# Kernel tuning notes

Measured on AMD Instinct MI355X. Metric: run time of the kernel, lower is better.

Reference implementation:

```python
import jax, jax.numpy as jnp
import numpy as np

SPACE = 63
STRIDE = 2
TEMP = 0.07
W_CHAR, W_WORD, W_PHRASE, W_IDEA = 1.0, 0.5, 0.1, 0.1


def setup_inputs() -> dict:
    key = jax.random.key(0)
    ks = jax.random.split(key, 6)
    B, S, V, D = 8, 4096, 256, 512
    return {
        "logits": jax.random.normal(ks[0], (B, S, V), jnp.float32),
        "word_preds": jax.random.normal(ks[1], (B, D, S // STRIDE), jnp.float32),
        "char_features": jax.random.normal(ks[2], (B, D, S), jnp.float32),
        "contrastive_2": jax.random.normal(ks[3], (B, 128, 1024), jnp.float32),
        "contrastive_3": jax.random.normal(ks[4], (B, 128, 256), jnp.float32),
        "targets": jax.random.randint(ks[5], (B, S), 0, V, jnp.int32),
        "mask": jnp.ones((B, S), jnp.float32),
    }


def _info_nce(emb, temp=TEMP):
    # emb: (B, dim, L). Anchors = even positions, positives = odd positions.
    B, dim, L = emb.shape
    n_pairs = L // 2
    a = emb[:, :, 0:2 * n_pairs:2].transpose(0, 2, 1).reshape(-1, dim)
    p = emb[:, :, 1:2 * n_pairs:2].transpose(0, 2, 1).reshape(-1, dim)
    a = a / jnp.maximum(jnp.linalg.norm(a, axis=1, keepdims=True), 1e-12)
    p = p / jnp.maximum(jnp.linalg.norm(p, axis=1, keepdims=True), 1e-12)
    logits = (a @ p.T) / temp  # (n, n)
    n = logits.shape[0]
    logp = jax.nn.log_softmax(logits, axis=1)
    idx = jnp.arange(n)
    return -jnp.mean(logp[idx, idx])


def _word_span_loss(word_preds, char_features, targets, stride=STRIDE):
    # Segment-mean over spans between consecutive spaces; MSE vs gathered preds.
    B, D, S = char_features.shape
    Wlen = word_preds.shape[2]
    nseg = S + 2  # segment k in [1, n_spaces-1] = span after the k-th space; last slot = junk
    space = targets == SPACE
    cs = jnp.cumsum(space.astype(jnp.int32), axis=1)  # inclusive space count
    seg = jnp.where(space, nseg - 1, cs)          # non-space chars -> span id
    seg_sp = jnp.where(space, cs, nseg - 1)       # space positions -> their space index k
    t_idx = jnp.arange(S, dtype=jnp.int32)

    def per_batch(feats, seg_b, seg_sp_b):
        sums = jax.ops.segment_sum(feats.T, seg_b, num_segments=nseg)  # (nseg, D)
        cnts = jax.ops.segment_sum(jnp.ones((S,), feats.dtype), seg_b, num_segments=nseg)
        pos = jnp.full((nseg,), S, jnp.int32).at[seg_sp_b].set(t_idx)  # position of k-th space
        return sums, cnts, pos

    sums, cnts, pos = jax.vmap(per_batch)(char_features, seg, seg_sp)
    n_sp = cs[:, -1]  # (B,)
    k = jnp.arange(nseg)[None, :]
    valid = (k >= 1) & (k <= n_sp[:, None] - 1) & (cnts > 0) & ((pos // stride) < Wlen)
    means = jax.lax.stop_gradient(sums / jnp.maximum(cnts, 1.0)[..., None])  # target.detach()
    wp = jnp.clip(pos // stride, 0, Wlen - 1)  # (B, nseg)
    preds = jnp.take_along_axis(word_preds.transpose(0, 2, 1), wp[:, :, None], axis=1)  # (B,nseg,D)
    mse = jnp.mean((preds - means) ** 2, axis=-1)  # per-span F.mse_loss (mean over feat dim)
    tot = jnp.sum(jnp.where(valid, mse, 0.0))
    cnt = jnp.sum(valid).astype(mse.dtype)
    return jnp.where(cnt > 0, tot / jnp.maximum(cnt, 1.0), 0.0)


def reference(logits, word_preds, char_features, contrastive_2, contrastive_3, targets, mask):
    # char CE with mask
    logp = jax.nn.log_softmax(logits, axis=-1)
    ce = -jnp.take_along_axis(logp, targets[..., None].astype(jnp.int32), axis=-1)[..., 0]
    n = jnp.sum(mask)
    char_loss = jnp.where(n > 0, jnp.sum(ce * mask) / jnp.maximum(n, 1.0), jnp.mean(ce))
    word_loss = _word_span_loss(word_preds, char_features, targets)
    phrase_loss = _info_nce(contrastive_2)
    idea_loss = _info_nce(contrastive_3)
    return (W_CHAR * char_loss + W_WORD * word_loss
            + W_PHRASE * phrase_loss + W_IDEA * idea_loss)
```

## Files before the change

kernel.cpp:

```cpp
#include <hip/hip_runtime.h>

#define SPACE_TOK 63
#define INV_T 14.285714285714286f
#define SA_SCALE 20.609929155556595f
#define LN2F 0.6931471805599453f

typedef __attribute__((ext_vector_type(8))) short bf16x8;
typedef __attribute__((ext_vector_type(4))) float f32x4;

#define O_CECM   0
#define O_CEM    4096
#define O_CEC    8192
#define O_WPART  12288
#define O_WCNT   14336
#define O_PEXP2  14464
#define O_DIAG2  145536
#define O_PEXP3  161920
#define O_DIAG3  194688
#define O_A2     198848
#define SZ_A2    (4096*128*2)
#define O_P2     (O_A2 + SZ_A2)
#define O_A3     (O_P2 + SZ_A2)
#define SZ_A3    (1024*128*2)
#define O_P3     (O_A3 + SZ_A3)

#define SMEM_A   18048
#define NTILE    4
#define SMEM_NCE (4*64*17*4 + 4*64*4)

__device__ inline unsigned short f2bf(float x) {
  union { float f; unsigned int u; } c; c.f = x;
  unsigned int r = c.u + 0x7fffu + ((c.u >> 16) & 1u);
  return (unsigned short)(r >> 16);
}

__device__ void norm_body(char* smem, const float* __restrict__ emb, int L,
                          unsigned short* __restrict__ Abf, unsigned short* __restrict__ Pbf,
                          int b, int l0) {
  float (*tile)[33] = (float(*)[33])smem;
  float (*np8)[32]  = (float(*)[32])(smem + 16896);
  float* scl        = (float*)(smem + 16896 + 1024);
  int tid = threadIdx.x;
  int lx = tid & 31, cq = tid >> 5;
  const float* eb = emb + (size_t)b * 128 * L + l0;
  for (int c = cq; c < 128; c += 8) tile[c][lx] = eb[(size_t)c * L + lx];
  __syncthreads();
  {
    float s = 0.f;
    for (int c = cq; c < 128; c += 8) { float x = tile[c][lx]; s += x * x; }
    np8[cq][lx] = s;
  }
  __syncthreads();
  if (tid < 32) {
    float t = 0.f;
#pragma unroll
    for (int g = 0; g < 8; ++g) t += np8[g][tid];
    float nrm = fmaxf(sqrtf(t), 1e-12f);
    scl[tid] = ((tid & 1) ? 1.0f : SA_SCALE) / nrm;
  }
  __syncthreads();
  int c = tid & 127, lh = tid >> 7;
  int half = L >> 1;
  int k = c >> 5, quad = (c >> 3) & 3, j = c & 7;
  for (int lp = lh; lp < 32; lp += 2) {
    int l = l0 + lp;
    int row = b * half + (l >> 1);
    unsigned short v = f2bf(tile[c][lp] * scl[lp]);
    unsigned short* dst = (l & 1) ? Pbf : Abf;
    dst[(size_t)(row >> 4) * 2048 + k * 512 + ((quad << 4) + (row & 15)) * 8 + j] = v;
  }
}

__device__ void word_body(char* smem, const float* __restrict__ wp,
                          const float* __restrict__ cf,
                          const int* __restrict__ targets,
                          char* __restrict__ ws, int w) {
  int* sc      = (int*)smem;
  int* splist  = (int*)(smem + 1024);
  int* snext_sh = (int*)(smem + 5120);
  float* wacc  = (float*)(smem + 5124);
  int tid = threadIdx.x;
  int z = w & 15, tq = (w >> 4) & 3, b = w >> 6;
  const int* tb = targets + b * 4096;
  int tbase = tq * 1024;
  int4 tok = ((const int4*)(tb + tbase))[tid];
  int f0 = (tok.x == SPACE_TOK), f1 = (tok.y == SPACE_TOK),
      f2 = (tok.z == SPACE_TOK), f3 = (tok.w == SPACE_TOK);
  int cnt = f0 + f1 + f2 + f3;
  sc[tid] = cnt;
  __syncthreads();
  for (int off = 1; off < 256; off <<= 1) {
    int v = (tid >= off) ? sc[tid - off] : 0;
    __syncthreads();
    sc[tid] += v;
    __syncthreads();
  }
  int base = sc[tid] - cnt;
  int p = tbase + tid * 4;
  if (f0) splist[base++] = p;
  if (f1) splist[base++] = p + 1;
  if (f2) splist[base++] = p + 2;
  if (f3) splist[base++] = p + 3;
  int m = sc[255];
  if (tid == 0) *snext_sh = -1;
  __syncthreads();
  if (m > 0) {
    for (int wstart = tbase + 1024; wstart < 4096 && *snext_sh < 0; wstart += 1024) {
      int t = wstart + tid * 4;
      int4 tk = ((const int4*)tb)[t >> 2];
      int found = 0x7fffffff;
      if (tk.x == SPACE_TOK) found = t;
      else if (tk.y == SPACE_TOK) found = t + 1;
      else if (tk.z == SPACE_TOK) found = t + 2;
      else if (tk.w == SPACE_TOK) found = t + 3;
#pragma unroll
      for (int mm = 1; mm < 64; mm <<= 1) found = min(found, __shfl_xor(found, mm));
      if ((tid & 63) == 0) sc[tid >> 6] = found;
      __syncthreads();
      if (tid == 0) {
        int f = min(min(sc[0], sc[1]), min(sc[2], sc[3]));
        if (f != 0x7fffffff) *snext_sh = f;
      }
      __syncthreads();
    }
  }
  int snext = *snext_sh;
  int wave = tid >> 6, lane = tid & 63;
  int dbase = z * 32 + wave * 8;
  const float* r0 = cf + ((size_t)(b * 512 + dbase)) * 4096;
  float myacc = 0.f;
  float lcnt = 0.f;
  for (int i = 0; i < m; ++i) {
    int t0 = splist[i];
    int t1 = (i + 1 < m) ? splist[i + 1] : snext;
    if (t1 < 0) break;
    int seglen = t1 - t0 - 1;
    if (seglen <= 0) continue;
    lcnt += 1.0f;
    int wpos = t0 >> 1;
    float invc = 1.0f / (float)seglen;
    float pred = 0.f;
    if (lane < 8) pred = wp[((size_t)(b * 512 + dbase + lane)) * 2048 + wpos];
    int c0 = (t0 + 1) >> 2;
    int c1 = (t1 + 3) >> 2;
    float s0 = 0.f, s1 = 0.f, s2 = 0.f, s3 = 0.f, s4 = 0.f, s5 = 0.f, s6 = 0.f, s7 = 0.f;
    for (int c = c0 + lane; c < c1; c += 64) {
      int tbp = c << 2;
      float4 v0 = *(const float4*)(r0 + 0 * 4096 + tbp);
      float4 v1 = *(const float4*)(r0 + 1 * 4096 + tbp);
      float4 v2 = *(const float4*)(r0 + 2 * 4096 + tbp);
      float4 v3 = *(const float4*)(r0 + 3 * 4096 + tbp);
      float4 v4 = *(const float4*)(r0 + 4 * 4096 + tbp);
      float4 v5 = *(const float4*)(r0 + 5 * 4096 + tbp);
      float4 v6 = *(const float4*)(r0 + 6 * 4096 + tbp);
      float4 v7 = *(const float4*)(r0 + 7 * 4096 + tbp);
      float m0 = (tbp + 0 > t0 && tbp + 0 < t1) ? 1.f : 0.f;
      float m1 = (tbp + 1 > t0 && tbp + 1 < t1) ? 1.f : 0.f;
      float m2 = (tbp + 2 > t0 && tbp + 2 < t1) ? 1.f : 0.f;
      float m3 = (tbp + 3 > t0 && tbp + 3 < t1) ? 1.f : 0.f;
      s0 += v0.x * m0 + v0.y * m1 + v0.z * m2 + v0.w * m3;
      s1 += v1.x * m0 + v1.y * m1 + v1.z * m2 + v1.w * m3;
      s2 += v2.x * m0 + v2.y * m1 + v2.z * m2 + v2.w * m3;
      s3 += v3.x * m0 + v3.y * m1 + v3.z * m2 + v3.w * m3;
      s4 += v4.x * m0 + v4.y * m1 + v4.z * m2 + v4.w * m3;
      s5 += v5.x * m0 + v5.y * m1 + v5.z * m2 + v5.w * m3;
      s6 += v6.x * m0 + v6.y * m1 + v6.z * m2 + v6.w * m3;
      s7 += v7.x * m0 + v7.y * m1 + v7.z * m2 + v7.w * m3;
    }
#pragma unroll
    for (int mm = 1; mm < 64; mm <<= 1) {
      s0 += __shfl_xor(s0, mm); s1 += __shfl_xor(s1, mm);
      s2 += __shfl_xor(s2, mm); s3 += __shfl_xor(s3, mm);
      s4 += __shfl_xor(s4, mm); s5 += __shfl_xor(s5, mm);
      s6 += __shfl_xor(s6, mm); s7 += __shfl_xor(s7, mm);
    }
    if (lane < 8) {
      float sv = (lane == 0) ? s0 : (lane == 1) ? s1 : (lane == 2) ? s2 : (lane == 3) ? s3
               : (lane == 4) ? s4 : (lane == 5) ? s5 : (lane == 6) ? s6 : s7;
      float mean = sv * invc;
      float diff = pred - mean;
      myacc += diff * diff;
    }
  }
#pragma unroll
  for (int mm = 1; mm < 8; mm <<= 1) myacc += __shfl_xor(myacc, mm);
  if (lane == 0) wacc[wave] = myacc;
  __syncthreads();
  if (tid == 0) {
    ((float*)(ws + O_WPART))[w] = (wacc[0] + wacc[1] + wacc[2] + wacc[3]) * (1.0f / 512.0f);
    if (z == 0) ((float*)(ws + O_WCNT))[w >> 4] = lcnt;
  }
}

__device__ void ce_body(char* smem, const float* __restrict__ logits,
                        const int* __restrict__ targets, const float* __restrict__ mask,
                        char* ws, int cb) {
  int tid = threadIdx.x;
  int wave = tid >> 6, lane = tid & 63;
  int rbase = cb * 32 + wave * 8;
  float4 v[8];
  float mk[8];
  int tg[8];
#pragma unroll
  for (int rr = 0; rr < 8; ++rr) v[rr] = ((const float4*)logits)[(size_t)(rbase + rr) * 64 + lane];
#pragma unroll
  for (int rr = 0; rr < 8; ++rr) { tg[rr] = targets[rbase + rr]; mk[rr] = mask[rbase + rr]; }
  float aCM = 0.f, aM = 0.f, aC = 0.f;
#pragma unroll
  for (int rr = 0; rr < 8; ++rr) {
    float e = __expf(v[rr].x) + __expf(v[rr].y) + __expf(v[rr].z) + __expf(v[rr].w);
#pragma unroll
    for (int m = 1; m < 64; m <<= 1) e += __shfl_xor(e, m);
    int t = tg[rr];
    int q = t & 3;
    float sel = (q == 0) ? v[rr].x : (q == 1) ? v[rr].y : (q == 2) ? v[rr].z : v[rr].w;
    float xt = __shfl(sel, t >> 2);
    float ce = __logf(e) - xt;
    aCM += ce * mk[rr]; aM += mk[rr]; aC += ce;
  }
  float (*red)[3] = (float(*)[3])smem;
  if (lane == 0) { red[wave][0] = aCM; red[wave][1] = aM; red[wave][2] = aC; }
  __syncthreads();
  if (tid == 0) {
    ((float*)(ws + O_CECM))[cb] = red[0][0] + red[1][0] + red[2][0] + red[3][0];
    ((float*)(ws + O_CEM ))[cb] = red[0][1] + red[1][1] + red[2][1] + red[3][1];
    ((float*)(ws + O_CEC ))[cb] = red[0][2] + red[1][2] + red[2][2] + red[3][2];
  }
}

__global__ void __launch_bounds__(256) fusedA_kernel(const float* __restrict__ logits,
                                                     const float* __restrict__ wp,
                                                     const float* __restrict__ cf,
                                                     const int* __restrict__ targets,
                                                     const float* __restrict__ mask,
                                                     const float* __restrict__ c2,
                                                     const float* __restrict__ c3,
                                                     char* __restrict__ ws) {
  extern __shared__ char smem[];
  int bid = blockIdx.x;
  if (bid < 512) {
    word_body(smem, wp, cf, targets, ws, bid);
  } else if (bid < 1536) {
    ce_body(smem, logits, targets, mask, ws, bid - 512);
  } else if (bid < 1792) {
    int nb = bid - 1536;
    norm_body(smem, c2, 1024, (unsigned short*)(ws + O_A2), (unsigned short*)(ws + O_P2),
              nb & 7, (nb >> 3) * 32);
  } else {
    int nb = bid - 1792;
    norm_body(smem, c3, 256, (unsigned short*)(ws + O_A3), (unsigned short*)(ws + O_P3),
              nb & 7, (nb >> 3) * 32);
  }
}

__device__ void nce_body(char* smem, const unsigned short* __restrict__ A,
                         const unsigned short* __restrict__ P, int sliceJ,
                         int grp, int s, float* __restrict__ pexp,
                         float* __restrict__ diag) {
  int tid = threadIdx.x;
  int wave = tid >> 6, lane = tid & 63;
  int col = lane & 15, quad = lane >> 4;
  int I0g = grp * (16 * NTILE);
  const unsigned short* At = A + (size_t)(I0g >> 4) * 2048 + lane * 8;
  bf16x8 a[NTILE][4];
#pragma unroll
  for (int t = 0; t < NTILE; ++t)
#pragma unroll
    for (int k = 0; k < 4; ++k)
      a[t][k] = *(const bf16x8*)(At + t * 2048 + k * 512);
  float rl[NTILE][4];
#pragma unroll
  for (int t = 0; t < NTILE; ++t)
#pragma unroll
    for (int q = 0; q < 4; ++q) rl[t][q] = 0.f;
  float dcap[NTILE];
#pragma unroll
  for (int t = 0; t < NTILE; ++t) dcap[t] = 0.f;
  int perW = sliceJ >> 2;
  int J0w = s * sliceJ + wave * perW, Jend = J0w + perW;
  for (int J = J0w; J < Jend; J += 16) {
    const unsigned short* Pt = P + (size_t)(J >> 4) * 2048 + lane * 8;
    bf16x8 b0 = *(const bf16x8*)(Pt);
    bf16x8 b1 = *(const bf16x8*)(Pt + 512);
    bf16x8 b2 = *(const bf16x8*)(Pt + 1024);
    bf16x8 b3 = *(const bf16x8*)(Pt + 1536);
#pragma unroll
    for (int t = 0; t < NTILE; ++t) {
      f32x4 cfr = {0.f, 0.f, 0.f, 0.f};
      cfr = __builtin_amdgcn_mfma_f32_16x16x32_bf16(a[t][0], b0, cfr, 0, 0, 0);
      cfr = __builtin_amdgcn_mfma_f32_16x16x32_bf16(a[t][1], b1, cfr, 0, 0, 0);
      cfr = __builtin_amdgcn_mfma_f32_16x16x32_bf16(a[t][2], b2, cfr, 0, 0, 0);
      cfr = __builtin_amdgcn_mfma_f32_16x16x32_bf16(a[t][3], b3, cfr, 0, 0, 0);
      rl[t][0] += exp2f(cfr[0] - SA_SCALE);
      rl[t][1] += exp2f(cfr[1] - SA_SCALE);
      rl[t][2] += exp2f(cfr[2] - SA_SCALE);
      rl[t][3] += exp2f(cfr[3] - SA_SCALE);
      if (J == I0g + 16 * t) {
        int r = col - (quad << 2);
        if (r == 0) dcap[t] = cfr[0];
        else if (r == 1) dcap[t] = cfr[1];
        else if (r == 2) dcap[t] = cfr[2];
        else if (r == 3) dcap[t] = cfr[3];
      }
    }
  }
  float (*part)[64][17] = (float(*)[64][17])smem;
  float (*dpart)[64]    = (float(*)[64])(smem + 18496);
#pragma unroll
  for (int t = 0; t < NTILE; ++t) {
    part[wave][t * 16 + (quad << 2) + 0][col] = rl[t][0];
    part[wave][t * 16 + (quad << 2) + 1][col] = rl[t][1];
    part[wave][t * 16 + (quad << 2) + 2][col] = rl[t][2];
    part[wave][t * 16 + (quad << 2) + 3][col] = rl[t][3];
    if (quad == (col >> 2)) dpart[wave][t * 16 + col] = dcap[t];
  }
  __syncthreads();
  {
    int rrow = tid >> 4, cc = tid & 15;
#pragma unroll
    for (int t = 0; t < NTILE; ++t) {
      int row = t * 16 + rrow;
      float sv = 0.f, d = 0.f;
#pragma unroll
      for (int ww = 0; ww < 4; ++ww) { sv += part[ww][row][cc]; d += dpart[ww][row]; }
#pragma unroll
      for (int mm = 1; mm < 16; mm <<= 1) sv += __shfl_xor(sv, mm);
      if (cc == 0) {
        int gi = I0g + row;
        pexp[gi] = sv;
        if (gi >= s * sliceJ && gi < (s + 1) * sliceJ) diag[gi] = d;
      }
    }
  }
}

__global__ void __launch_bounds__(256) nce_kernel(char* __restrict__ ws) {
  extern __shared__ char smem[];
  int bid = blockIdx.x;
  if (bid < 512) {
    nce_body(smem, (const unsigned short*)(ws + O_A2), (const unsigned short*)(ws + O_P2),
             512, bid >> 3, bid & 7,
             (float*)(ws + O_PEXP2) + (bid & 7) * 4096, (float*)(ws + O_DIAG2));
  } else {
    int nb = bid - 512;
    nce_body(smem, (const unsigned short*)(ws + O_A3), (const unsigned short*)(ws + O_P3),
             128, nb >> 3, nb & 7,
             (float*)(ws + O_PEXP3) + (nb & 7) * 1024, (float*)(ws + O_DIAG3));
  }
}

__global__ void __launch_bounds__(256) final_kernel(const char* __restrict__ ws,
                                                    float* __restrict__ out) {
  int tid = threadIdx.x;
  int wave = tid >> 6, lane = tid & 63;
  float v[7] = {0.f, 0.f, 0.f, 0.f, 0.f, 0.f, 0.f};
  {
    float4 a = ((const float4*)(ws + O_CECM))[tid];
    float4 bb = ((const float4*)(ws + O_CEM))[tid];
    float4 c = ((const float4*)(ws + O_CEC))[tid];
    v[0] = a.x + a.y + a.z + a.w;
    v[1] = bb.x + bb.y + bb.z + bb.w;
    v[2] = c.x + c.y + c.z + c.w;
  }
  if (tid < 128) {
    float4 wv = ((const float4*)(ws + O_WPART))[tid];
    v[3] = wv.x + wv.y + wv.z + wv.w;
  }
  if (tid < 32) v[4] = ((const float*)(ws + O_WCNT))[tid];
  for (int r4 = tid; r4 < 1024; r4 += 256) {
    float4 S = {0.f, 0.f, 0.f, 0.f};
#pragma unroll
    for (int s = 0; s < 8; ++s) {
      float4 pv = ((const float4*)(ws + O_PEXP2))[s * 1024 + r4];
      S.x += pv.x; S.y += pv.y; S.z += pv.z; S.w += pv.w;
    }
    float4 dg = ((const float4*)(ws + O_DIAG2))[r4];
    v[5] += 4.0f * INV_T + __logf(S.x) + __logf(S.y) + __logf(S.z) + __logf(S.w)
            - LN2F * (dg.x + dg.y + dg.z + dg.w);
  }
  {
    int r4 = tid;
    float4 S = {0.f, 0.f, 0.f, 0.f};
#pragma unroll
    for (int s = 0; s < 8; ++s) {
      float4 pv = ((const float4*)(ws + O_PEXP3))[s * 256 + r4];
      S.x += pv.x; S.y += pv.y; S.z += pv.z; S.w += pv.w;
    }
    float4 dg = ((const float4*)(ws + O_DIAG3))[r4];
    v[6] = 4.0f * INV_T + __logf(S.x) + __logf(S.y) + __logf(S.z) + __logf(S.w)
           - LN2F * (dg.x + dg.y + dg.z + dg.w);
  }
#pragma unroll
  for (int j = 0; j < 7; ++j) {
    float x = v[j];
#pragma unroll
    for (int mm = 1; mm < 64; mm <<= 1) x += __shfl_xor(x, mm);
    v[j] = x;
  }
  __shared__ float fr[4][7];
  if (lane == 0)
#pragma unroll
    for (int j = 0; j < 7; ++j) fr[wave][j] = v[j];
  __syncthreads();
  if (tid == 0) {
    float s[7];
#pragma unroll
    for (int j = 0; j < 7; ++j) s[j] = fr[0][j] + fr[1][j] + fr[2][j] + fr[3][j];
    float n = s[1];
    float charL = (n > 0.f) ? (s[0] / fmaxf(n, 1.f)) : (s[2] / 32768.0f);
    float wordL = (s[4] > 0.f) ? (s[3] / fmaxf(s[4], 1.f)) : 0.f;
    out[0] = charL + 0.5f * wordL + 0.1f * (s[5] / 4096.0f) + 0.1f * (s[6] / 1024.0f);
  }
}

extern "C" void kernel_launch(void* const* d_in, const int* in_sizes, int n_in,
                              void* d_out, int out_size, void* d_ws, size_t ws_size,
                              hipStream_t stream) {
  (void)in_sizes; (void)n_in; (void)out_size; (void)ws_size;
  const float* logits        = (const float*)d_in[0];
  const float* word_preds    = (const float*)d_in[1];
  const float* char_features = (const float*)d_in[2];
  const float* c2            = (const float*)d_in[3];
  const float* c3            = (const float*)d_in[4];
  const int*   targets       = (const int*)d_in[5];
  const float* mask          = (const float*)d_in[6];
  float* out = (float*)d_out;
  char* ws = (char*)d_ws;

  fusedA_kernel<<<1856, 256, SMEM_A, stream>>>(logits, word_preds, char_features,
                                               targets, mask, c2, c3, ws);
  nce_kernel<<<640, 256, SMEM_NCE, stream>>>(ws);
  final_kernel<<<1, 256, 0, stream>>>(ws, out);
}
```

Baseline: 173.7 us.

## Split word-span loss into separate 1024-thread kernel, spread segments over waves

Moves the word-span segment-mean work out of the fused kernel into its own launch with 1024 threads per block. The 16 waves now split the span list four ways, each group of four waves taking every fourth segment, which shortens the serial per-block segment loop. The fused kernel keeps only the cross-entropy and normalization blocks. This adds one kernel launch and serializes the word work ahead of the CE and norm blocks, where before they overlapped in a single grid.

```diff
diff --git a/kernel.cpp b/kernel.cpp
--- a/kernel.cpp
+++ b/kernel.cpp
@@ -34,106 +34,81 @@
   return (unsigned short)(r >> 16);
 }
 
-__device__ void norm_body(char* smem, const float* __restrict__ emb, int L,
-                          unsigned short* __restrict__ Abf, unsigned short* __restrict__ Pbf,
-                          int b, int l0) {
-  float (*tile)[33] = (float(*)[33])smem;
-  float (*np8)[32]  = (float(*)[32])(smem + 16896);
-  float* scl        = (float*)(smem + 16896 + 1024);
+__global__ void __launch_bounds__(1024) word_kernel(const float* __restrict__ wp,
+                                                    const float* __restrict__ cf,
+                                                    const int* __restrict__ targets,
+                                                    char* __restrict__ ws) {
+  __shared__ int sc[256];
+  __shared__ int splist[1024];
+  __shared__ int snext_sh;
+  __shared__ float wacc[16];
+  __shared__ float lcw[16];
   int tid = threadIdx.x;
-  int lx = tid & 31, cq = tid >> 5;
-  const float* eb = emb + (size_t)b * 128 * L + l0;
-  for (int c = cq; c < 128; c += 8) tile[c][lx] = eb[(size_t)c * L + lx];
-  __syncthreads();
-  {
-    float s = 0.f;
-    for (int c = cq; c < 128; c += 8) { float x = tile[c][lx]; s += x * x; }
-    np8[cq][lx] = s;
-  }
-  __syncthreads();
-  if (tid < 32) {
-    float t = 0.f;
-#pragma unroll
-    for (int g = 0; g < 8; ++g) t += np8[g][tid];
-    float nrm = fmaxf(sqrtf(t), 1e-12f);
-    scl[tid] = ((tid & 1) ? 1.0f : SA_SCALE) / nrm;
-  }
-  __syncthreads();
-  int c = tid & 127, lh = tid >> 7;
-  int half = L >> 1;
-  int k = c >> 5, quad = (c >> 3) & 3, j = c & 7;
-  for (int lp = lh; lp < 32; lp += 2) {
-    int l = l0 + lp;
-    int row = b * half + (l >> 1);
-    unsigned short v = f2bf(tile[c][lp] * scl[lp]);
-    unsigned short* dst = (l & 1) ? Pbf : Abf;
-    dst[(size_t)(row >> 4) * 2048 + k * 512 + ((quad << 4) + (row & 15)) * 8 + j] = v;
-  }
-}
-
-__device__ void word_body(char* smem, const float* __restrict__ wp,
-                          const float* __restrict__ cf,
-                          const int* __restrict__ targets,
-                          char* __restrict__ ws, int w) {
-  int* sc      = (int*)smem;
-  int* splist  = (int*)(smem + 1024);
-  int* snext_sh = (int*)(smem + 5120);
-  float* wacc  = (float*)(smem + 5124);
-  int tid = threadIdx.x;
+  int w = blockIdx.x;
   int z = w & 15, tq = (w >> 4) & 3, b = w >> 6;
   const int* tb = targets + b * 4096;
   int tbase = tq * 1024;
-  int4 tok = ((const int4*)(tb + tbase))[tid];
-  int f0 = (tok.x == SPACE_TOK), f1 = (tok.y == SPACE_TOK),
-      f2 = (tok.z == SPACE_TOK), f3 = (tok.w == SPACE_TOK);
-  int cnt = f0 + f1 + f2 + f3;
-  sc[tid] = cnt;
+
+  int cnt = 0, f0 = 0, f1 = 0, f2 = 0, f3 = 0;
+  if (tid < 256) {
+    int4 tok = ((const int4*)(tb + tbase))[tid];
+    f0 = (tok.x == SPACE_TOK); f1 = (tok.y == SPACE_TOK);
+    f2 = (tok.z == SPACE_TOK); f3 = (tok.w == SPACE_TOK);
+    cnt = f0 + f1 + f2 + f3;
+    sc[tid] = cnt;
+  }
   __syncthreads();
   for (int off = 1; off < 256; off <<= 1) {
-    int v = (tid >= off) ? sc[tid - off] : 0;
+    int v = (tid >= off && tid < 256) ? sc[tid - off] : 0;
     __syncthreads();
-    sc[tid] += v;
+    if (tid < 256) sc[tid] += v;
     __syncthreads();
   }
-  int base = sc[tid] - cnt;
-  int p = tbase + tid * 4;
-  if (f0) splist[base++] = p;
-  if (f1) splist[base++] = p + 1;
-  if (f2) splist[base++] = p + 2;
-  if (f3) splist[base++] = p + 3;
+  if (tid < 256) {
+    int base = sc[tid] - cnt;
+    int p4 = tbase + tid * 4;
+    if (f0) splist[base++] = p4;
+    if (f1) splist[base++] = p4 + 1;
+    if (f2) splist[base++] = p4 + 2;
+    if (f3) splist[base++] = p4 + 3;
+  }
   int m = sc[255];
-  if (tid == 0) *snext_sh = -1;
+  if (tid == 0) snext_sh = -1;
   __syncthreads();
   if (m > 0) {
-    for (int wstart = tbase + 1024; wstart < 4096 && *snext_sh < 0; wstart += 1024) {
-      int t = wstart + tid * 4;
-      int4 tk = ((const int4*)tb)[t >> 2];
+    for (int wstart = tbase + 1024; wstart < 4096 && snext_sh < 0; wstart += 1024) {
       int found = 0x7fffffff;
-      if (tk.x == SPACE_TOK) found = t;
-      else if (tk.y == SPACE_TOK) found = t + 1;
-      else if (tk.z == SPACE_TOK) found = t + 2;
-      else if (tk.w == SPACE_TOK) found = t + 3;
-#pragma unroll
-      for (int mm = 1; mm < 64; mm <<= 1) found = min(found, __shfl_xor(found, mm));
-      if ((tid & 63) == 0) sc[tid >> 6] = found;
+      if (tid < 256) {
+        int t = wstart + tid * 4;
+        int4 tk = ((const int4*)tb)[t >> 2];
+        if (tk.x == SPACE_TOK) found = t;
+        else if (tk.y == SPACE_TOK) found = t + 1;
+        else if (tk.z == SPACE_TOK) found = t + 2;
+        else if (tk.w == SPACE_TOK) found = t + 3;
+#pragma unroll
+        for (int mm = 1; mm < 64; mm <<= 1) found = min(found, __shfl_xor(found, mm));
+        if ((tid & 63) == 0) sc[tid >> 6] = found;
+      }
       __syncthreads();
       if (tid == 0) {
         int f = min(min(sc[0], sc[1]), min(sc[2], sc[3]));
-        if (f != 0x7fffffff) *snext_sh = f;
+        if (f != 0x7fffffff) snext_sh = f;
       }
       __syncthreads();
     }
   }
-  int snext = *snext_sh;
+  int snext = snext_sh;
+
   int wave = tid >> 6, lane = tid & 63;
-  int dbase = z * 32 + wave * 8;
+  int g = wave & 3, p = wave >> 2;
+  int dbase = z * 32 + g * 8;
   const float* r0 = cf + ((size_t)(b * 512 + dbase)) * 4096;
   float myacc = 0.f;
   float lcnt = 0.f;
-  for (int i = 0; i < m; ++i) {
+  for (int i = p; i < m; i += 4) {
     int t0 = splist[i];
     int t1 = (i + 1 < m) ? splist[i + 1] : snext;
-    if (t1 < 0) break;
+    if (t1 < 0) continue;
     int seglen = t1 - t0 - 1;
     if (seglen <= 0) continue;
     lcnt += 1.0f;
@@ -184,11 +159,51 @@
   }
 #pragma unroll
   for (int mm = 1; mm < 8; mm <<= 1) myacc += __shfl_xor(myacc, mm);
-  if (lane == 0) wacc[wave] = myacc;
+  if (lane == 0) { wacc[wave] = myacc; lcw[wave] = lcnt; }
   __syncthreads();
   if (tid == 0) {
-    ((float*)(ws + O_WPART))[w] = (wacc[0] + wacc[1] + wacc[2] + wacc[3]) * (1.0f / 512.0f);
-    if (z == 0) ((float*)(ws + O_WCNT))[w >> 4] = lcnt;
+    float s = 0.f;
+#pragma unroll
+    for (int ww = 0; ww < 16; ++ww) s += wacc[ww];
+    ((float*)(ws + O_WPART))[w] = s * (1.0f / 512.0f);
+    if (z == 0) ((float*)(ws + O_WCNT))[w >> 4] = lcw[0] + lcw[4] + lcw[8] + lcw[12];
+  }
+}
+
+__device__ void norm_body(char* smem, const float* __restrict__ emb, int L,
+                          unsigned short* __restrict__ Abf, unsigned short* __restrict__ Pbf,
+                          int b, int l0) {
+  float (*tile)[33] = (float(*)[33])smem;
+  float (*np8)[32]  = (float(*)[32])(smem + 16896);
+  float* scl        = (float*)(smem + 16896 + 1024);
+  int tid = threadIdx.x;
+  int lx = tid & 31, cq = tid >> 5;
+  const float* eb = emb + (size_t)b * 128 * L + l0;
+  for (int c = cq; c < 128; c += 8) tile[c][lx] = eb[(size_t)c * L + lx];
+  __syncthreads();
+  {
+    float s = 0.f;
+    for (int c = cq; c < 128; c += 8) { float x = tile[c][lx]; s += x * x; }
+    np8[cq][lx] = s;
+  }
+  __syncthreads();
+  if (tid < 32) {
+    float t = 0.f;
+#pragma unroll
+    for (int g = 0; g < 8; ++g) t += np8[g][tid];
+    float nrm = fmaxf(sqrtf(t), 1e-12f);
+    scl[tid] = ((tid & 1) ? 1.0f : SA_SCALE) / nrm;
+  }
+  __syncthreads();
+  int c = tid & 127, lh = tid >> 7;
+  int half = L >> 1;
+  int k = c >> 5, quad = (c >> 3) & 3, j = c & 7;
+  for (int lp = lh; lp < 32; lp += 2) {
+    int l = l0 + lp;
+    int row = b * half + (l >> 1);
+    unsigned short v = f2bf(tile[c][lp] * scl[lp]);
+    unsigned short* dst = (l & 1) ? Pbf : Abf;
+    dst[(size_t)(row >> 4) * 2048 + k * 512 + ((quad << 4) + (row & 15)) * 8 + j] = v;
   }
 }
 
@@ -229,8 +244,6 @@
 }
 
 __global__ void __launch_bounds__(256) fusedA_kernel(const float* __restrict__ logits,
-                                                     const float* __restrict__ wp,
-                                                     const float* __restrict__ cf,
                                                      const int* __restrict__ targets,
                                                      const float* __restrict__ mask,
                                                      const float* __restrict__ c2,
@@ -238,16 +251,14 @@
                                                      char* __restrict__ ws) {
   extern __shared__ char smem[];
   int bid = blockIdx.x;
-  if (bid < 512) {
-    word_body(smem, wp, cf, targets, ws, bid);
-  } else if (bid < 1536) {
-    ce_body(smem, logits, targets, mask, ws, bid - 512);
-  } else if (bid < 1792) {
-    int nb = bid - 1536;
+  if (bid < 1024) {
+    ce_body(smem, logits, targets, mask, ws, bid);
+  } else if (bid < 1280) {
+    int nb = bid - 1024;
     norm_body(smem, c2, 1024, (unsigned short*)(ws + O_A2), (unsigned short*)(ws + O_P2),
               nb & 7, (nb >> 3) * 32);
   } else {
-    int nb = bid - 1792;
+    int nb = bid - 1280;
     norm_body(smem, c3, 256, (unsigned short*)(ws + O_A3), (unsigned short*)(ws + O_P3),
               nb & 7, (nb >> 3) * 32);
   }
@@ -427,8 +438,8 @@
   float* out = (float*)d_out;
   char* ws = (char*)d_ws;
 
-  fusedA_kernel<<<1856, 256, SMEM_A, stream>>>(logits, word_preds, char_features,
-                                               targets, mask, c2, c3, ws);
+  word_kernel<<<512, 1024, 0, stream>>>(word_preds, char_features, targets, ws);
+  fusedA_kernel<<<1344, 256, SMEM_A, stream>>>(logits, targets, mask, c2, c3, ws);
   nce_kernel<<<640, 256, SMEM_NCE, stream>>>(ws);
   final_kernel<<<1, 256, 0, stream>>>(ws, out);
 }
```

Measured after the change: 178.0 us. +2.5%, slower.
